# Optimization experiments

Hardware: AMD Instinct MI355X
Metric: run time of the kernel (lower is better)

## Reference

```python
import jax, jax.numpy as jnp
import numpy as np

HEAD_SIZE = 64
EPS_GN = 1e-5 * 8 * 8  # GroupNorm eps = 1e-5 * head_size_divisor**2


def rwkv7_scan(w_raw, q, k, v, a, b):
    """RWKV-7 'wind backstepping' linear recurrence.
    Inputs [B,T,H,N]. Per step (matching the CUDA kernel):
      decay = exp(-exp(w_raw)); sa = S @ a; S = S*decay + sa b^T + v k^T; y = S @ q
    State S is [B,H,N_value,N_key]."""
    decay = jnp.exp(-jnp.exp(w_raw))
    B, T, H, N = q.shape
    xs = tuple(jnp.moveaxis(t, 1, 0) for t in (decay, q, k, v, a, b))  # [T,B,H,N]
    S0 = jnp.zeros((B, H, N, N), q.dtype)

    def step(S, inp):
        d, qt, kt, vt, at, bt = inp
        sa = jnp.einsum('bhij,bhj->bhi', S, at)
        S = S * d[:, :, None, :] + sa[..., None] * bt[:, :, None, :] + vt[..., None] * kt[:, :, None, :]
        y = jnp.einsum('bhij,bhj->bhi', S, qt)
        return S, y

    _, ys = jax.lax.scan(step, S0, xs)
    return jnp.moveaxis(ys, 0, 1)  # [B,T,H,N]


def setup_inputs() -> dict:
    key = jax.random.key(0)
    B, T, C, H, N = 4, 960, 2048, 32, 64
    Dw, Da, Dv, Dg = 96, 96, 64, 256
    ks = iter(jax.random.split(key, 40))

    def nrm(shape, s=0.02):
        return jax.random.normal(next(ks), shape, jnp.float32) * s

    def uni(shape):
        return jax.random.uniform(next(ks), shape, jnp.float32)

    return dict(
        x=nrm((B, T, C), 1.0),
        v_first=nrm((B, T, C), 1.0),
        x_r=uni((1, 1, C)), x_w=uni((1, 1, C)), x_k=uni((1, 1, C)),
        x_v=uni((1, 1, C)), x_a=uni((1, 1, C)), x_g=uni((1, 1, C)),
        w0=jnp.linspace(-7.0, -2.0, C, dtype=jnp.float32).reshape(1, 1, C) + 0.5,
        w1=nrm((C, Dw)), w2=nrm((Dw, C)),
        a0=nrm((1, 1, C)), a1=nrm((C, Da)), a2=nrm((Da, C)),
        v0=jnp.ones((1, 1, C), jnp.float32), v1=nrm((C, Dv)), v2=nrm((Dv, C)),
        g1=nrm((C, Dg)), g2=nrm((Dg, C)),
        k_k=jnp.full((1, 1, C), 0.85, jnp.float32),
        k_a=jnp.ones((1, 1, C), jnp.float32),
        r_k=nrm((H, N)),
        Wr=nrm((C, C)), Wk=nrm((C, C)), Wv=nrm((C, C)), Wo=nrm((C, C)),
        ln_w=jnp.ones((C,), jnp.float32), ln_b=jnp.zeros((C,), jnp.float32),
    )


def reference(x, v_first, x_r, x_w, x_k, x_v, x_a, x_g,
              w0, w1, w2, a0, a1, a2, v0, v1, v2, g1, g2,
              k_k, k_a, r_k, Wr, Wk, Wv, Wo, ln_w, ln_b):
    B, T, C = x.shape
    H = C // HEAD_SIZE
    # time_shift: ZeroPad2d((0,0,1,-1)) == shift right by 1 along T with zero at t=0
    x_prev = jnp.pad(x, ((0, 0), (1, 0), (0, 0)))[:, :T]
    xx = x_prev - x
    xr = x + xx * x_r; xw = x + xx * x_w; xk = x + xx * x_k
    xv = x + xx * x_v; xa = x + xx * x_a; xg = x + xx * x_g

    r = xr @ Wr.T
    w = -jax.nn.softplus(-(w0 + jnp.tanh(xw @ w1) @ w2)) - 0.5
    k = xk @ Wk.T
    v = xv @ Wv.T
    # layer_id != 0: residual-value mixing with first layer's value
    v = v + (v_first - v) * jax.nn.sigmoid(v0 + (xv @ v1) @ v2)
    a = jax.nn.sigmoid(a0 + (xa @ a1) @ a2)
    g = jax.nn.sigmoid(xg @ g1) @ g2

    kk = (k * k_k).reshape(B, T, H, HEAD_SIZE)
    kk = kk / jnp.maximum(jnp.linalg.norm(kk, axis=-1, keepdims=True), 1e-12)  # F.normalize
    kk = kk.reshape(B, T, C)
    k = k * (1 + (a - 1) * k_a)

    hs = lambda t: t.reshape(B, T, H, HEAD_SIZE)
    y = rwkv7_scan(hs(w), hs(r), hs(k), hs(v), hs(-kk), hs(kk * a)).reshape(B, T, C)

    # GroupNorm(H groups over C)
    yg = y.reshape(B, T, H, HEAD_SIZE)
    mu = yg.mean(-1, keepdims=True)
    var = yg.var(-1, keepdims=True)
    y = ((yg - mu) / jnp.sqrt(var + EPS_GN)).reshape(B, T, C) * ln_w + ln_b

    y = y + ((hs(r) * hs(k) * r_k).sum(-1, keepdims=True) * hs(v)).reshape(B, T, C)
    return (y * g) @ Wo.T
```

## Files before the change

kernel.cpp:

```cpp
#include <hip/hip_runtime.h>
#include <stdint.h>

#define BDIM 4
#define TDIM 960
#define CDIM 2048
#define HDIM 32
#define NDIM 64
#define BT   (BDIM*TDIM)

typedef unsigned short u16;
typedef __attribute__((ext_vector_type(8))) short short8;
typedef __attribute__((ext_vector_type(4))) float f32x4;

__device__ __forceinline__ float b2f(u16 u){
  union{unsigned int i; float f;}x; x.i=((unsigned int)u)<<16; return x.f;
}
__device__ __forceinline__ u16 f2b(float f){
  union{float f; unsigned int i;}x; x.f=f;
  unsigned int r = x.i + 0x7fffu + ((x.i>>16)&1u);
  return (u16)(r>>16);
}
__device__ __forceinline__ void unpack8(uint4 p, float* o){
  o[0]=b2f((u16)(p.x&0xffff)); o[1]=b2f((u16)(p.x>>16));
  o[2]=b2f((u16)(p.y&0xffff)); o[3]=b2f((u16)(p.y>>16));
  o[4]=b2f((u16)(p.z&0xffff)); o[5]=b2f((u16)(p.z>>16));
  o[6]=b2f((u16)(p.w&0xffff)); o[7]=b2f((u16)(p.w>>16));
}
__device__ __forceinline__ uint4 pack8(const float* o){
  uint4 p;
  p.x = (unsigned)f2b(o[0]) | ((unsigned)f2b(o[1])<<16);
  p.y = (unsigned)f2b(o[2]) | ((unsigned)f2b(o[3])<<16);
  p.z = (unsigned)f2b(o[4]) | ((unsigned)f2b(o[5])<<16);
  p.w = (unsigned)f2b(o[6]) | ((unsigned)f2b(o[7])<<16);
  return p;
}
__device__ __forceinline__ void ld8f(const float* p, float* o){
  float4 a = *(const float4*)p;
  float4 b = *(const float4*)(p+4);
  o[0]=a.x;o[1]=a.y;o[2]=a.z;o[3]=a.w;o[4]=b.x;o[5]=b.y;o[6]=b.z;o[7]=b.w;
}
__device__ __forceinline__ float sigm(float x){ return 1.f/(1.f+expf(-x)); }
__device__ __forceinline__ void stc(float* p, float v){ *p = v; }
__device__ __forceinline__ void stc(u16* p, float v){ *p = f2b(v); }

__device__ __forceinline__ float row_red16(float x){
  x += __int_as_float(__builtin_amdgcn_update_dpp(0, __float_as_int(x), 0xB1,  0xF, 0xF, true));
  x += __int_as_float(__builtin_amdgcn_update_dpp(0, __float_as_int(x), 0x4E,  0xF, 0xF, true));
  x += __int_as_float(__builtin_amdgcn_update_dpp(0, __float_as_int(x), 0x141, 0xF, 0xF, true));
  x += __int_as_float(__builtin_amdgcn_update_dpp(0, __float_as_int(x), 0x140, 0xF, 0xF, true));
  return x;
}

__global__ __launch_bounds__(256) void cvt_kernel(const float* src, u16* dst){
  size_t i = ((size_t)blockIdx.x*256 + threadIdx.x)*8;
  float v[8]; ld8f(src+i, v);
  *(uint4*)(dst+i) = pack8(v);
}

struct TJob { const float* src; u16* dst; int R, Cs, DR, DC; };
struct TJobs8 { TJob j[8]; };

__global__ __launch_bounds__(256) void transpose_pad_kernel(TJobs8 jobs){
  TJob jb = jobs.j[blockIdx.z];
  int idx = blockIdx.x*256 + threadIdx.x;
  int total = jb.DR*jb.DC;
  if (idx >= total) return;
  int i = idx / jb.DC, k = idx % jb.DC;
  float v = 0.f;
  if (i < jb.Cs && k < jb.R) v = jb.src[(size_t)k*jb.Cs + i];
  jb.dst[idx] = f2b(v);
}

__global__ __launch_bounds__(256) void mix_kernel(
  const float* x,
  const float* cr, const float* cw, const float* ck,
  const float* cv, const float* ca, const float* cg,
  u16* mr, u16* mw, u16* mk, u16* mv, u16* ma, u16* mg)
{
  size_t tid = (size_t)blockIdx.x*256 + threadIdx.x;
  size_t base = tid*8;
  int c = (int)(base % CDIM);
  int row = (int)(base / CDIM);
  int t = row % TDIM;
  float xc[8], xp[8], xx[8], cf[8], o[8];
  ld8f(x+base, xc);
  if (t > 0) {
    ld8f(x+base-CDIM, xp);
  } else {
    for(int j=0;j<8;j++) xp[j]=0.f;
  }
  #pragma unroll
  for(int j=0;j<8;j++) xx[j]=xp[j]-xc[j];
#define DOMIX(CP, OP) do { ld8f(CP+c, cf); \
  _Pragma("unroll") for(int j=0;j<8;j++) o[j]=xc[j]+xx[j]*cf[j]; \
  *(uint4*)(OP+base)=pack8(o); } while(0)
  DOMIX(cr, mr); DOMIX(cw, mw); DOMIX(ck, mk);
  DOMIX(cv, mv); DOMIX(ca, ma); DOMIX(cg, mg);
#undef DOMIX
}

struct GemmJob {
  const u16* A; const u16* Bt; void* C;
  int nbm, nbn, K, lda, ldb, ldc;
};
struct GemmJobs { GemmJob j[4]; };

template<typename TC>
__global__ __launch_bounds__(256, 2) void gemm_bt_kernel(GemmJobs jobs){
  GemmJob jb = jobs.j[blockIdx.z];
  int bm = blockIdx.x % jb.nbm;
  int bn = blockIdx.x / jb.nbm;
  if (bn >= jb.nbn) return;
  __shared__ __attribute__((aligned(16))) u16 As[128*64];
  __shared__ __attribute__((aligned(16))) u16 Bs[128*64];
  int tid = threadIdx.x;
  int wave = tid>>6, lane = tid&63;
  int wr = wave>>1, wc = wave&1;
  f32x4 acc[4][4];
  #pragma unroll
  for(int i=0;i<4;i++)
    #pragma unroll
    for(int j=0;j<4;j++) acc[i][j] = (f32x4){0.f,0.f,0.f,0.f};
  const int rA0 = bm*128;
  const int rB0 = bn*128;
  int srow = (lane>>3);
  int scol = (lane&7)*8;
  for (int k0=0; k0<jb.K; k0+=64){
    #pragma unroll
    for (int it=0; it<4; ++it){
      int rr = wave*32 + it*8;
      const u16* gA = jb.A + (size_t)(rA0 + rr + srow)*jb.lda + (k0 + scol);
      __builtin_amdgcn_global_load_lds((const __attribute__((address_space(1))) void*)gA,
          (__attribute__((address_space(3))) void*)&As[rr*64], 16, 0, 0);
      const u16* gB = jb.Bt + (size_t)(rB0 + rr + srow)*jb.ldb + (k0 + scol);
      __builtin_amdgcn_global_load_lds((const __attribute__((address_space(1))) void*)gB,
          (__attribute__((address_space(3))) void*)&Bs[rr*64], 16, 0, 0);
    }
    __syncthreads();
    #pragma unroll
    for (int kc=0; kc<2; ++kc){
      short8 af[4], bfr[4];
      int ko = kc*32 + (lane>>4)*8;
      #pragma unroll
      for (int mi=0; mi<4; ++mi)
        af[mi] = *(const short8*)&As[(wr*64 + mi*16 + (lane&15))*64 + ko];
      #pragma unroll
      for (int ni=0; ni<4; ++ni)
        bfr[ni] = *(const short8*)&Bs[(wc*64 + ni*16 + (lane&15))*64 + ko];
      #pragma unroll
      for (int mi=0; mi<4; ++mi)
        #pragma unroll
        for (int ni=0; ni<4; ++ni)
          acc[mi][ni] = __builtin_amdgcn_mfma_f32_16x16x32_bf16(af[mi], bfr[ni], acc[mi][ni], 0, 0, 0);
    }
    __syncthreads();
  }
  TC* C = (TC*)jb.C;
  int cn = (lane&15);
  int rq = (lane>>4)*4;
  #pragma unroll
  for (int mi=0; mi<4; ++mi){
    #pragma unroll
    for (int ni=0; ni<4; ++ni){
      int col = rB0 + wc*64 + ni*16 + cn;
      int row = rA0 + wr*64 + mi*16 + rq;
      #pragma unroll
      for (int e=0; e<4; ++e)
        stc(&C[(size_t)(row+e)*jb.ldc + col], acc[mi][ni][e]);
    }
  }
}

__global__ __launch_bounds__(256) void act_kernel(u16* hw, u16* hg){
  int idx = blockIdx.x*256 + threadIdx.x;
  if (blockIdx.z==0){ if (idx < BT*128) hw[idx] = f2b(tanhf(b2f(hw[idx]))); }
  else              { if (idx < BT*256) hg[idx] = f2b(sigm(b2f(hg[idx]))); }
}

__global__ __launch_bounds__(256) void post_kernel(
  const u16* kbuf, const u16* vraw, const float* vfirst,
  const u16* wl, const u16* al, const u16* vl,
  const float* w0, const float* a0, const float* v0,
  const float* kkc, const float* kac,
  float* dout, u16* ks, u16* vs, u16* as_, u16* bs)
{
  int row = blockIdx.x, tid = threadIdx.x;
  int c = tid*8;
  size_t base = (size_t)row*CDIM + c;
  float kf[8], vr[8], vf[8], wlf[8], alf[8], vlf[8], w0f[8], a0f[8], v0f[8], kkf[8], kaf[8];
  unpack8(*(const uint4*)(kbuf+base), kf);
  unpack8(*(const uint4*)(vraw+base), vr);
  ld8f(vfirst+base, vf);
  unpack8(*(const uint4*)(wl+base), wlf);
  unpack8(*(const uint4*)(al+base), alf);
  unpack8(*(const uint4*)(vl+base), vlf);
  ld8f(w0+c, w0f);
  ld8f(a0+c, a0f);
  ld8f(v0+c, v0f);
  ld8f(kkc+c, kkf);
  ld8f(kac+c, kaf);
  float dv[8], av[8], vv[8], kkr[8], kfin[8], asv[8], bsv[8];
  float ssq = 0.f;
  #pragma unroll
  for (int j=0;j<8;j++){
    float wv = -log1pf(expf(-(w0f[j]+wlf[j]))) - 0.5f;
    dv[j]  = expf(-expf(wv));
    av[j]  = sigm(a0f[j]+alf[j]);
    vv[j]  = vr[j] + (vf[j]-vr[j])*sigm(v0f[j]+vlf[j]);
    kkr[j] = kf[j]*kkf[j];
    ssq   += kkr[j]*kkr[j];
    kfin[j]= kf[j]*(1.f + (av[j]-1.f)*kaf[j]);
  }
  ssq += __shfl_xor(ssq,1); ssq += __shfl_xor(ssq,2); ssq += __shfl_xor(ssq,4);
  float inv = 1.f/fmaxf(sqrtf(ssq), 1e-12f);
  #pragma unroll
  for (int j=0;j<8;j++){ float kkn = kkr[j]*inv; asv[j] = -kkn; bsv[j] = kkn*av[j]; }
  *(float4*)(dout+base)   = make_float4(dv[0],dv[1],dv[2],dv[3]);
  *(float4*)(dout+base+4) = make_float4(dv[4],dv[5],dv[6],dv[7]);
  *(uint4*)(ks+base)  = pack8(kfin);
  *(uint4*)(vs+base)  = pack8(vv);
  *(uint4*)(as_+base) = pack8(asv);
  *(uint4*)(bs+base)  = pack8(bsv);
}

__global__ __launch_bounds__(256, 2) void scan_kernel(
  const float* __restrict__ decayp, const u16* __restrict__ qb,
  const u16* __restrict__ kb, const u16* __restrict__ vb,
  const u16* __restrict__ ab, const u16* __restrict__ bb,
  float* __restrict__ yb)
{
  int blk = blockIdx.x;
  int b    = blk >> 7;
  int h    = (blk >> 2) & 31;
  int qtr  = blk & 3;
  int tid = threadIdx.x;
  int jg = tid & 15;
  int ii = tid >> 4;
  int row = qtr*16 + ii;
  size_t hbase = ((size_t)b*TDIM)*CDIM + (size_t)h*NDIM;

  const float* dp = decayp + hbase + jg*4;
  const u16*  qp = qb + hbase + jg*4;
  const u16*  kp = kb + hbase + jg*4;
  const u16*  ap = ab + hbase + jg*4;
  const u16*  bp = bb + hbase + jg*4;
  const u16*  vp = vb + hbase + row;

  float S[4] = {0.f, 0.f, 0.f, 0.f};

  struct StepRegs { f32x4 d; ushort4 q, k, a, b; u16 v; };
  auto loadstep = [&](int t)->StepRegs{
    StepRegs r;
    size_t off = (size_t)t*CDIM;
    r.d = *(const f32x4*)(dp + off);
    r.q = *(const ushort4*)(qp + off);
    r.k = *(const ushort4*)(kp + off);
    r.a = *(const ushort4*)(ap + off);
    r.b = *(const ushort4*)(bp + off);
    r.v = vp[off];
    return r;
  };
  auto dostep = [&](const StepRegs& r)->float{
    float a0=b2f(r.a.x), a1=b2f(r.a.y), a2=b2f(r.a.z), a3=b2f(r.a.w);
    float sap = (S[0]*a0 + S[1]*a1) + (S[2]*a2 + S[3]*a3);
    sap = row_red16(sap);
    float k0=b2f(r.k.x), k1=b2f(r.k.y), k2=b2f(r.k.z), k3=b2f(r.k.w);
    float c0=b2f(r.b.x), c1=b2f(r.b.y), c2=b2f(r.b.z), c3=b2f(r.b.w);
    float vi=b2f(r.v);
    S[0] = S[0]*r.d[0] + sap*c0 + vi*k0;
    S[1] = S[1]*r.d[1] + sap*c1 + vi*k1;
    S[2] = S[2]*r.d[2] + sap*c2 + vi*k2;
    S[3] = S[3]*r.d[3] + sap*c3 + vi*k3;
    return (S[0]*b2f(r.q.x) + S[1]*b2f(r.q.y)) + (S[2]*b2f(r.q.z) + S[3]*b2f(r.q.w));
  };

  StepRegs R0 = loadstep(0), R1 = loadstep(1), R2 = loadstep(2), R3 = loadstep(3);
  for (int g=0; g<120; ++g){
    float yp[8];
#define STEP(RR, S_) { int t_ = g*8 + (S_); int tn_ = t_+4 < TDIM ? t_+4 : TDIM-1; \
    StepRegs nn_ = loadstep(tn_); yp[S_] = dostep(RR); RR = nn_; }
    STEP(R0,0) STEP(R1,1) STEP(R2,2) STEP(R3,3)
    STEP(R0,4) STEP(R1,5) STEP(R2,6) STEP(R3,7)
#undef STEP
    #pragma unroll
    for (int s=0; s<8; ++s) yp[s] = row_red16(yp[s]);
    if (jg < 8){
      float out = 0.f;
      #pragma unroll
      for (int s=0; s<8; ++s) if (jg==s) out = yp[s];
      yb[hbase + (size_t)(g*8+jg)*CDIM + row] = out;
    }
  }
}

__global__ __launch_bounds__(256) void final_kernel(
  const float* yb, const u16* rb, const u16* ks, const u16* vs,
  const float* rk, const float* lnw, const float* lnb, const u16* gl, u16* yg)
{
  int row = blockIdx.x, tid = threadIdx.x;
  int c = tid*8;
  size_t base = (size_t)row*CDIM + c;
  float y[8], rf[8], kf[8], vf[8], rkf[8], lw[8], lb[8], gf[8];
  ld8f(yb+base, y);
  unpack8(*(const uint4*)(rb+base), rf);
  unpack8(*(const uint4*)(ks+base), kf);
  unpack8(*(const uint4*)(vs+base), vf);
  ld8f(rk+c,  rkf);
  ld8f(lnw+c, lw);
  ld8f(lnb+c, lb);
  unpack8(*(const uint4*)(gl+base), gf);
  float sy=0.f, syy=0.f, coef=0.f;
  #pragma unroll
  for (int j=0;j<8;j++){ sy+=y[j]; syy+=y[j]*y[j]; coef += rf[j]*kf[j]*rkf[j]; }
  sy  += __shfl_xor(sy,1);  sy  += __shfl_xor(sy,2);  sy  += __shfl_xor(sy,4);
  syy += __shfl_xor(syy,1); syy += __shfl_xor(syy,2); syy += __shfl_xor(syy,4);
  coef+= __shfl_xor(coef,1);coef+= __shfl_xor(coef,2);coef+= __shfl_xor(coef,4);
  float mu  = sy*(1.f/64.f);
  float var = syy*(1.f/64.f) - mu*mu;
  float rs  = rsqrtf(var + 6.4e-4f);
  float o[8];
  #pragma unroll
  for (int j=0;j<8;j++)
    o[j] = (((y[j]-mu)*rs)*lw[j] + lb[j] + coef*vf[j]) * gf[j];
  *(uint4*)(yg+base) = pack8(o);
}

extern "C" void kernel_launch(void* const* d_in, const int* in_sizes, int n_in,
                              void* d_out, int out_size, void* d_ws, size_t ws_size,
                              hipStream_t stream)
{
  const float* x      = (const float*)d_in[0];
  const float* vfirst = (const float*)d_in[1];
  const float* c_r = (const float*)d_in[2];
  const float* c_w = (const float*)d_in[3];
  const float* c_k = (const float*)d_in[4];
  const float* c_v = (const float*)d_in[5];
  const float* c_a = (const float*)d_in[6];
  const float* c_g = (const float*)d_in[7];
  const float* w0i = (const float*)d_in[8];
  const float* w1i = (const float*)d_in[9];
  const float* w2i = (const float*)d_in[10];
  const float* a0i = (const float*)d_in[11];
  const float* a1i = (const float*)d_in[12];
  const float* a2i = (const float*)d_in[13];
  const float* v0i = (const float*)d_in[14];
  const float* v1i = (const float*)d_in[15];
  const float* v2i = (const float*)d_in[16];
  const float* g1i = (const float*)d_in[17];
  const float* g2i = (const float*)d_in[18];
  const float* kki = (const float*)d_in[19];
  const float* kai = (const float*)d_in[20];
  const float* rki = (const float*)d_in[21];
  const float* Wr  = (const float*)d_in[22];
  const float* Wk  = (const float*)d_in[23];
  const float* Wv  = (const float*)d_in[24];
  const float* Wo  = (const float*)d_in[25];
  const float* lnw = (const float*)d_in[26];
  const float* lnb = (const float*)d_in[27];

  char* ws = (char*)d_ws;
  const size_t S2 = (size_t)BT*CDIM*2;
  u16* MIXR = (u16*)(ws + 0*S2);
  u16* MIXW = (u16*)(ws + 1*S2);
  u16* MIXK = (u16*)(ws + 2*S2);
  u16* MIXV = (u16*)(ws + 3*S2);
  u16* MIXA = (u16*)(ws + 4*S2);
  u16* MIXG = (u16*)(ws + 5*S2);
  u16* RBUF = (u16*)(ws + 6*S2);
  u16* KBUF = (u16*)(ws + 7*S2);
  u16* VRAW = (u16*)(ws + 8*S2);
  char* WB = ws + 9*S2;
  u16* WSLOT = (u16*)WB;
  char* WT = WB + 8388608;
  u16* W1T = (u16*)(WT + 0);
  u16* A1T = (u16*)(WT + 524288);
  u16* V1T = (u16*)(WT + 1048576);
  u16* G1T = (u16*)(WT + 1572864);
  u16* W2T = (u16*)(WT + 2621440);
  u16* A2T = (u16*)(WT + 3145728);
  u16* V2T = (u16*)(WT + 3670016);
  u16* G2T = (u16*)(WT + 4194304);
  char* HB = WT + 5242880;
  u16* HW = (u16*)(HB + 0);
  u16* HA = (u16*)(HB + 983040);
  u16* HV = (u16*)(HB + 1966080);
  u16* HG = (u16*)(HB + 2949120);
  char* L2 = HB + 4915200;
  u16* WL = (u16*)(L2 + 0*S2);
  u16* AL = (u16*)(L2 + 1*S2);
  u16* VL = (u16*)(L2 + 2*S2);
  u16* GL = (u16*)(L2 + 3*S2);
  float* WDEC = (float*)(ws + 0*S2);
  u16* KS = (u16*)(ws + 2*S2);
  u16* VS = (u16*)(ws + 3*S2);
  u16* AS = (u16*)(ws + 4*S2);
  u16* BS = (u16*)(ws + 5*S2);
  float* YBUF = (float*)(L2 + 0*S2);
  u16* YG = (u16*)(L2 + 2*S2);
  (void)in_sizes; (void)n_in; (void)out_size; (void)ws_size;

  TJobs8 tj;
  tj.j[0] = (TJob){w1i, W1T, 2048,  96, 128, 2048};
  tj.j[1] = (TJob){a1i, A1T, 2048,  96, 128, 2048};
  tj.j[2] = (TJob){v1i, V1T, 2048,  64, 128, 2048};
  tj.j[3] = (TJob){g1i, G1T, 2048, 256, 256, 2048};
  tj.j[4] = (TJob){w2i, W2T,   96, 2048, 2048, 128};
  tj.j[5] = (TJob){a2i, A2T,   96, 2048, 2048, 128};
  tj.j[6] = (TJob){v2i, V2T,   64, 2048, 2048, 128};
  tj.j[7] = (TJob){g2i, G2T,  256, 2048, 2048, 256};
  transpose_pad_kernel<<<dim3(2048,1,8), 256, 0, stream>>>(tj);

  mix_kernel<<<dim3(BT*CDIM/8/256), 256, 0, stream>>>(
      x, c_r, c_w, c_k, c_v, c_a, c_g, MIXR, MIXW, MIXK, MIXV, MIXA, MIXG);

  {
    GemmJobs gj;
    cvt_kernel<<<dim3(2048), 256, 0, stream>>>(Wr, WSLOT);
    gj.j[0] = (GemmJob){MIXR, WSLOT, RBUF, 30, 16, 2048, 2048, 2048, 2048};
    gj.j[1] = gj.j[0]; gj.j[2] = gj.j[0]; gj.j[3] = gj.j[0];
    gemm_bt_kernel<u16><<<dim3(480,1,1), 256, 0, stream>>>(gj);
    cvt_kernel<<<dim3(2048), 256, 0, stream>>>(Wk, WSLOT);
    gj.j[0] = (GemmJob){MIXK, WSLOT, KBUF, 30, 16, 2048, 2048, 2048, 2048};
    gemm_bt_kernel<u16><<<dim3(480,1,1), 256, 0, stream>>>(gj);
    cvt_kernel<<<dim3(2048), 256, 0, stream>>>(Wv, WSLOT);
    gj.j[0] = (GemmJob){MIXV, WSLOT, VRAW, 30, 16, 2048, 2048, 2048, 2048};
    gemm_bt_kernel<u16><<<dim3(480,1,1), 256, 0, stream>>>(gj);
  }

  GemmJobs lj1;
  lj1.j[0] = (GemmJob){MIXW, W1T, HW, 30, 1, 2048, 2048, 2048, 128};
  lj1.j[1] = (GemmJob){MIXA, A1T, HA, 30, 1, 2048, 2048, 2048, 128};
  lj1.j[2] = (GemmJob){MIXV, V1T, HV, 30, 1, 2048, 2048, 2048, 128};
  lj1.j[3] = (GemmJob){MIXG, G1T, HG, 30, 2, 2048, 2048, 2048, 256};
  gemm_bt_kernel<u16><<<dim3(60,1,4), 256, 0, stream>>>(lj1);

  act_kernel<<<dim3(3840,1,2), 256, 0, stream>>>(HW, HG);

  GemmJobs lj2;
  lj2.j[0] = (GemmJob){HW, W2T, WL, 30, 16, 128, 128, 128, 2048};
  lj2.j[1] = (GemmJob){HA, A2T, AL, 30, 16, 128, 128, 128, 2048};
  lj2.j[2] = (GemmJob){HV, V2T, VL, 30, 16, 128, 128, 128, 2048};
  lj2.j[3] = (GemmJob){HG, G2T, GL, 30, 16, 256, 256, 256, 2048};
  gemm_bt_kernel<u16><<<dim3(480,1,4), 256, 0, stream>>>(lj2);

  post_kernel<<<dim3(BT), 256, 0, stream>>>(
      KBUF, VRAW, vfirst, WL, AL, VL, w0i, a0i, v0i, kki, kai,
      WDEC, KS, VS, AS, BS);

  scan_kernel<<<dim3(512), 256, 0, stream>>>(
      WDEC, RBUF, KS, VS, AS, BS, YBUF);

  final_kernel<<<dim3(BT), 256, 0, stream>>>(
      YBUF, RBUF, KS, VS, rki, lnw, lnb, GL, YG);

  cvt_kernel<<<dim3(2048), 256, 0, stream>>>(Wo, WSLOT);
  GemmJobs oj;
  oj.j[0] = (GemmJob){YG, WSLOT, d_out, 30, 16, 2048, 2048, 2048, 2048};
  oj.j[1] = oj.j[0]; oj.j[2] = oj.j[0]; oj.j[3] = oj.j[0];
  gemm_bt_kernel<float><<<dim3(480,1,1), 256, 0, stream>>>(oj);
}
```

Baseline: 897.7 us.

## Split scan state across 32 lanes per row and interleave a/b vectors

The scan kernel now gives each thread two state columns instead of four, with 32 lanes per state row and 8 rows per block. The grid doubles to 1024 blocks and occupancy is raised to 4 blocks per CU. The a and b vectors are written by post_kernel in an interleaved layout, so one 8-byte load fetches both. This shortens the serial per-step work and exposes more parallelism in the latency-bound recurrence, at the cost of an extra cross-half shuffle per reduction and more redundant loads of the shared vectors.

```diff
diff --git a/kernel.cpp b/kernel.cpp
--- a/kernel.cpp
+++ b/kernel.cpp
@@ -182,7 +182,7 @@
   const u16* wl, const u16* al, const u16* vl,
   const float* w0, const float* a0, const float* v0,
   const float* kkc, const float* kac,
-  float* dout, u16* ks, u16* vs, u16* as_, u16* bs)
+  float* dout, u16* ks, u16* vs, uint2* abi)
 {
   int row = blockIdx.x, tid = threadIdx.x;
   int c = tid*8;
@@ -219,59 +219,62 @@
   *(float4*)(dout+base+4) = make_float4(dv[4],dv[5],dv[6],dv[7]);
   *(uint4*)(ks+base)  = pack8(kfin);
   *(uint4*)(vs+base)  = pack8(vv);
-  *(uint4*)(as_+base) = pack8(asv);
-  *(uint4*)(bs+base)  = pack8(bsv);
-}
-
-__global__ __launch_bounds__(256, 2) void scan_kernel(
+  uint2* abe = abi + (size_t)row*1024 + (size_t)(c>>6)*32 + ((c&63)>>1);
+  #pragma unroll
+  for (int m=0;m<4;m++)
+    abe[m] = make_uint2((unsigned)f2b(asv[2*m]) | ((unsigned)f2b(asv[2*m+1])<<16),
+                        (unsigned)f2b(bsv[2*m]) | ((unsigned)f2b(bsv[2*m+1])<<16));
+}
+
+__global__ __launch_bounds__(256, 4) void scan_kernel(
   const float* __restrict__ decayp, const u16* __restrict__ qb,
   const u16* __restrict__ kb, const u16* __restrict__ vb,
-  const u16* __restrict__ ab, const u16* __restrict__ bb,
-  float* __restrict__ yb)
+  const uint2* __restrict__ abi, float* __restrict__ yb)
 {
   int blk = blockIdx.x;
-  int b    = blk >> 7;
-  int h    = (blk >> 2) & 31;
-  int qtr  = blk & 3;
+  int b   = blk >> 8;
+  int h   = (blk >> 3) & 31;
+  int oct = blk & 7;
   int tid = threadIdx.x;
-  int jg = tid & 15;
-  int ii = tid >> 4;
-  int row = qtr*16 + ii;
+  int jg  = tid & 31;
+  int ii  = tid >> 5;
+  int row = oct*8 + ii;
   size_t hbase = ((size_t)b*TDIM)*CDIM + (size_t)h*NDIM;
 
-  const float* dp = decayp + hbase + jg*4;
-  const u16*  qp = qb + hbase + jg*4;
-  const u16*  kp = kb + hbase + jg*4;
-  const u16*  ap = ab + hbase + jg*4;
-  const u16*  bp = bb + hbase + jg*4;
-  const u16*  vp = vb + hbase + row;
-
-  float S[4] = {0.f, 0.f, 0.f, 0.f};
-
-  struct StepRegs { f32x4 d; ushort4 q, k, a, b; u16 v; };
+  const char* dU = (const char*)(decayp + hbase);
+  const char* qU = (const char*)(qb + hbase);
+  const char* kU = (const char*)(kb + hbase);
+  const char* vU = (const char*)(vb + hbase);
+  const char* aU = (const char*)(abi + (size_t)b*TDIM*1024 + (size_t)h*32);
+
+  unsigned o8 = (unsigned)(jg*8);
+  unsigned o4 = (unsigned)(jg*4);
+  unsigned ov = (unsigned)(row*2);
+
+  float Sx = 0.f, Sy = 0.f;
+
+  struct StepRegs { float2 d; uint2 ab; unsigned q, k; u16 v; };
   auto loadstep = [&](int t)->StepRegs{
     StepRegs r;
-    size_t off = (size_t)t*CDIM;
-    r.d = *(const f32x4*)(dp + off);
-    r.q = *(const ushort4*)(qp + off);
-    r.k = *(const ushort4*)(kp + off);
-    r.a = *(const ushort4*)(ap + off);
-    r.b = *(const ushort4*)(bp + off);
-    r.v = vp[off];
+    unsigned t8 = (unsigned)t*8192u, t4 = (unsigned)t*4096u;
+    r.d  = *(const float2*)  (dU + (o8 + t8));
+    r.ab = *(const uint2*)   (aU + (o8 + t8));
+    r.q  = *(const unsigned*)(qU + (o4 + t4));
+    r.k  = *(const unsigned*)(kU + (o4 + t4));
+    r.v  = *(const u16*)     (vU + (ov + t4));
     return r;
   };
   auto dostep = [&](const StepRegs& r)->float{
-    float a0=b2f(r.a.x), a1=b2f(r.a.y), a2=b2f(r.a.z), a3=b2f(r.a.w);
-    float sap = (S[0]*a0 + S[1]*a1) + (S[2]*a2 + S[3]*a3);
+    float aLo = b2f((u16)(r.ab.x & 0xffff)), aHi = b2f((u16)(r.ab.x >> 16));
+    float sap = Sx*aLo + Sy*aHi;
     sap = row_red16(sap);
-    float k0=b2f(r.k.x), k1=b2f(r.k.y), k2=b2f(r.k.z), k3=b2f(r.k.w);
-    float c0=b2f(r.b.x), c1=b2f(r.b.y), c2=b2f(r.b.z), c3=b2f(r.b.w);
-    float vi=b2f(r.v);
-    S[0] = S[0]*r.d[0] + sap*c0 + vi*k0;
-    S[1] = S[1]*r.d[1] + sap*c1 + vi*k1;
-    S[2] = S[2]*r.d[2] + sap*c2 + vi*k2;
-    S[3] = S[3]*r.d[3] + sap*c3 + vi*k3;
-    return (S[0]*b2f(r.q.x) + S[1]*b2f(r.q.y)) + (S[2]*b2f(r.q.z) + S[3]*b2f(r.q.w));
+    sap += __shfl_xor(sap, 16);
+    float bLo = b2f((u16)(r.ab.y & 0xffff)), bHi = b2f((u16)(r.ab.y >> 16));
+    float kLo = b2f((u16)(r.k & 0xffff)),    kHi = b2f((u16)(r.k >> 16));
+    float vi  = b2f(r.v);
+    Sx = Sx*r.d.x + sap*bLo + vi*kLo;
+    Sy = Sy*r.d.y + sap*bHi + vi*kHi;
+    return Sx*b2f((u16)(r.q & 0xffff)) + Sy*b2f((u16)(r.q >> 16));
   };
 
   StepRegs R0 = loadstep(0), R1 = loadstep(1), R2 = loadstep(2), R3 = loadstep(3);
@@ -283,7 +286,10 @@
     STEP(R0,4) STEP(R1,5) STEP(R2,6) STEP(R3,7)
 #undef STEP
     #pragma unroll
-    for (int s=0; s<8; ++s) yp[s] = row_red16(yp[s]);
+    for (int s=0; s<8; ++s){
+      yp[s] = row_red16(yp[s]);
+      yp[s] += __shfl_xor(yp[s], 16);
+    }
     if (jg < 8){
       float out = 0.f;
       #pragma unroll
@@ -393,8 +399,7 @@
   float* WDEC = (float*)(ws + 0*S2);
   u16* KS = (u16*)(ws + 2*S2);
   u16* VS = (u16*)(ws + 3*S2);
-  u16* AS = (u16*)(ws + 4*S2);
-  u16* BS = (u16*)(ws + 5*S2);
+  uint2* ABI = (uint2*)(ws + 4*S2);
   float* YBUF = (float*)(L2 + 0*S2);
   u16* YG = (u16*)(L2 + 2*S2);
   (void)in_sizes; (void)n_in; (void)out_size; (void)ws_size;
@@ -445,10 +450,10 @@
 
   post_kernel<<<dim3(BT), 256, 0, stream>>>(
       KBUF, VRAW, vfirst, WL, AL, VL, w0i, a0i, v0i, kki, kai,
-      WDEC, KS, VS, AS, BS);
-
-  scan_kernel<<<dim3(512), 256, 0, stream>>>(
-      WDEC, RBUF, KS, VS, AS, BS, YBUF);
+      WDEC, KS, VS, ABI);
+
+  scan_kernel<<<dim3(1024), 256, 0, stream>>>(
+      WDEC, RBUF, KS, VS, ABI, YBUF);
 
   final_kernel<<<dim3(BT), 256, 0, stream>>>(
       YBUF, RBUF, KS, VS, rki, lnw, lnb, GL, YG);
```

Result: slower. 932.7 us (+3.9%).

## Interleave q/k and a/b into packed buffers and deepen scan prefetch

Applied to the files above, without the earlier changes.

The post kernel now writes q and k interleaved into one buffer and a and b into another, so each scan step issues fewer, wider loads (two 16-byte loads instead of four 8-byte loads). The scan prefetch depth grows from 4 to 8 steps, and sched_barriers split each 8-step group into pairs of steps. The final kernel reads r and k from the interleaved buffer. The aim is to cut load instruction count and hide latency in the serial scan, at the cost of more registers and an extra r read in post_kernel.

```diff
diff --git a/kernel.cpp b/kernel.cpp
--- a/kernel.cpp
+++ b/kernel.cpp
@@ -20,6 +20,9 @@
   unsigned int r = x.i + 0x7fffu + ((x.i>>16)&1u);
   return (u16)(r>>16);
 }
+__device__ __forceinline__ unsigned pk2(float lo, float hi){
+  return (unsigned)f2b(lo) | ((unsigned)f2b(hi)<<16);
+}
 __device__ __forceinline__ void unpack8(uint4 p, float* o){
   o[0]=b2f((u16)(p.x&0xffff)); o[1]=b2f((u16)(p.x>>16));
   o[2]=b2f((u16)(p.y&0xffff)); o[3]=b2f((u16)(p.y>>16));
@@ -28,10 +31,10 @@
 }
 __device__ __forceinline__ uint4 pack8(const float* o){
   uint4 p;
-  p.x = (unsigned)f2b(o[0]) | ((unsigned)f2b(o[1])<<16);
-  p.y = (unsigned)f2b(o[2]) | ((unsigned)f2b(o[3])<<16);
-  p.z = (unsigned)f2b(o[4]) | ((unsigned)f2b(o[5])<<16);
-  p.w = (unsigned)f2b(o[6]) | ((unsigned)f2b(o[7])<<16);
+  p.x = pk2(o[0],o[1]);
+  p.y = pk2(o[2],o[3]);
+  p.z = pk2(o[4],o[5]);
+  p.w = pk2(o[6],o[7]);
   return p;
 }
 __device__ __forceinline__ void ld8f(const float* p, float* o){
@@ -178,16 +181,17 @@
 }
 
 __global__ __launch_bounds__(256) void post_kernel(
-  const u16* kbuf, const u16* vraw, const float* vfirst,
+  const u16* rbuf, const u16* kbuf, const u16* vraw, const float* vfirst,
   const u16* wl, const u16* al, const u16* vl,
   const float* w0, const float* a0, const float* v0,
   const float* kkc, const float* kac,
-  float* dout, u16* ks, u16* vs, u16* as_, u16* bs)
+  float* dout, uint4* qki, uint4* abi, u16* vs)
 {
   int row = blockIdx.x, tid = threadIdx.x;
   int c = tid*8;
   size_t base = (size_t)row*CDIM + c;
-  float kf[8], vr[8], vf[8], wlf[8], alf[8], vlf[8], w0f[8], a0f[8], v0f[8], kkf[8], kaf[8];
+  float qf[8], kf[8], vr[8], vf[8], wlf[8], alf[8], vlf[8], w0f[8], a0f[8], v0f[8], kkf[8], kaf[8];
+  unpack8(*(const uint4*)(rbuf+base), qf);
   unpack8(*(const uint4*)(kbuf+base), kf);
   unpack8(*(const uint4*)(vraw+base), vr);
   ld8f(vfirst+base, vf);
@@ -217,84 +221,87 @@
   for (int j=0;j<8;j++){ float kkn = kkr[j]*inv; asv[j] = -kkn; bsv[j] = kkn*av[j]; }
   *(float4*)(dout+base)   = make_float4(dv[0],dv[1],dv[2],dv[3]);
   *(float4*)(dout+base+4) = make_float4(dv[4],dv[5],dv[6],dv[7]);
-  *(uint4*)(ks+base)  = pack8(kfin);
-  *(uint4*)(vs+base)  = pack8(vv);
-  *(uint4*)(as_+base) = pack8(asv);
-  *(uint4*)(bs+base)  = pack8(bsv);
+  uint4* qke = (uint4*)((char*)qki + (size_t)row*8192 + (size_t)c*4);
+  qke[0] = make_uint4(pk2(qf[0],qf[1]), pk2(kfin[0],kfin[1]), pk2(qf[2],qf[3]), pk2(kfin[2],kfin[3]));
+  qke[1] = make_uint4(pk2(qf[4],qf[5]), pk2(kfin[4],kfin[5]), pk2(qf[6],qf[7]), pk2(kfin[6],kfin[7]));
+  uint4* abe = (uint4*)((char*)abi + (size_t)row*8192 + (size_t)c*4);
+  abe[0] = make_uint4(pk2(asv[0],asv[1]), pk2(bsv[0],bsv[1]), pk2(asv[2],asv[3]), pk2(bsv[2],bsv[3]));
+  abe[1] = make_uint4(pk2(asv[4],asv[5]), pk2(bsv[4],bsv[5]), pk2(asv[6],asv[7]), pk2(bsv[6],bsv[7]));
+  *(uint4*)(vs+base) = pack8(vv);
 }
 
 __global__ __launch_bounds__(256, 2) void scan_kernel(
-  const float* __restrict__ decayp, const u16* __restrict__ qb,
-  const u16* __restrict__ kb, const u16* __restrict__ vb,
-  const u16* __restrict__ ab, const u16* __restrict__ bb,
+  const float* __restrict__ decayp, const uint4* __restrict__ qki,
+  const uint4* __restrict__ abi, const u16* __restrict__ vs,
   float* __restrict__ yb)
 {
   int blk = blockIdx.x;
   int b    = blk >> 7;
   int h    = (blk >> 2) & 31;
   int qtr  = blk & 3;
-  int tid = threadIdx.x;
-  int jg = tid & 15;
-  int ii = tid >> 4;
-  int row = qtr*16 + ii;
-  size_t hbase = ((size_t)b*TDIM)*CDIM + (size_t)h*NDIM;
-
-  const float* dp = decayp + hbase + jg*4;
-  const u16*  qp = qb + hbase + jg*4;
-  const u16*  kp = kb + hbase + jg*4;
-  const u16*  ap = ab + hbase + jg*4;
-  const u16*  bp = bb + hbase + jg*4;
-  const u16*  vp = vb + hbase + row;
-
-  float S[4] = {0.f, 0.f, 0.f, 0.f};
-
-  struct StepRegs { f32x4 d; ushort4 q, k, a, b; u16 v; };
-  auto loadstep = [&](int t)->StepRegs{
-    StepRegs r;
-    size_t off = (size_t)t*CDIM;
-    r.d = *(const f32x4*)(dp + off);
-    r.q = *(const ushort4*)(qp + off);
-    r.k = *(const ushort4*)(kp + off);
-    r.a = *(const ushort4*)(ap + off);
-    r.b = *(const ushort4*)(bp + off);
-    r.v = vp[off];
+  int tid  = threadIdx.x;
+  int jg   = tid & 15;
+  int ii   = tid >> 4;
+  int row  = qtr*16 + ii;
+
+  const char* dP = (const char*)decayp + (size_t)b*TDIM*8192 + h*256 + jg*16;
+  const char* qP = (const char*)qki    + (size_t)b*TDIM*8192 + h*256 + jg*16;
+  const char* aP = (const char*)abi    + (size_t)b*TDIM*8192 + h*256 + jg*16;
+  const char* vP = (const char*)vs     + (size_t)b*TDIM*4096 + h*128 + row*2;
+
+  float S0=0.f, S1=0.f, S2=0.f, S3=0.f;
+
+  struct SR { f32x4 d; uint4 qk; uint4 ab; u16 v; };
+  auto ld = [&](int t)->SR{
+    SR r; size_t o = (size_t)t*8192;
+    r.d  = *(const f32x4*)(dP + o);
+    r.qk = *(const uint4*)(qP + o);
+    r.ab = *(const uint4*)(aP + o);
+    r.v  = *(const u16*)(vP + (size_t)t*4096);
     return r;
   };
-  auto dostep = [&](const StepRegs& r)->float{
-    float a0=b2f(r.a.x), a1=b2f(r.a.y), a2=b2f(r.a.z), a3=b2f(r.a.w);
-    float sap = (S[0]*a0 + S[1]*a1) + (S[2]*a2 + S[3]*a3);
+  auto dostep = [&](const SR& r)->float{
+    float a0=b2f((u16)(r.ab.x&0xffff)), a1=b2f((u16)(r.ab.x>>16));
+    float a2=b2f((u16)(r.ab.z&0xffff)), a3=b2f((u16)(r.ab.z>>16));
+    float sap = (S0*a0 + S1*a1) + (S2*a2 + S3*a3);
     sap = row_red16(sap);
-    float k0=b2f(r.k.x), k1=b2f(r.k.y), k2=b2f(r.k.z), k3=b2f(r.k.w);
-    float c0=b2f(r.b.x), c1=b2f(r.b.y), c2=b2f(r.b.z), c3=b2f(r.b.w);
+    float c0=b2f((u16)(r.ab.y&0xffff)), c1=b2f((u16)(r.ab.y>>16));
+    float c2=b2f((u16)(r.ab.w&0xffff)), c3=b2f((u16)(r.ab.w>>16));
+    float k0=b2f((u16)(r.qk.y&0xffff)), k1=b2f((u16)(r.qk.y>>16));
+    float k2=b2f((u16)(r.qk.w&0xffff)), k3=b2f((u16)(r.qk.w>>16));
     float vi=b2f(r.v);
-    S[0] = S[0]*r.d[0] + sap*c0 + vi*k0;
-    S[1] = S[1]*r.d[1] + sap*c1 + vi*k1;
-    S[2] = S[2]*r.d[2] + sap*c2 + vi*k2;
-    S[3] = S[3]*r.d[3] + sap*c3 + vi*k3;
-    return (S[0]*b2f(r.q.x) + S[1]*b2f(r.q.y)) + (S[2]*b2f(r.q.z) + S[3]*b2f(r.q.w));
+    S0 = S0*r.d[0] + sap*c0 + vi*k0;
+    S1 = S1*r.d[1] + sap*c1 + vi*k1;
+    S2 = S2*r.d[2] + sap*c2 + vi*k2;
+    S3 = S3*r.d[3] + sap*c3 + vi*k3;
+    return (S0*b2f((u16)(r.qk.x&0xffff)) + S1*b2f((u16)(r.qk.x>>16)))
+         + (S2*b2f((u16)(r.qk.z&0xffff)) + S3*b2f((u16)(r.qk.z>>16)));
   };
 
-  StepRegs R0 = loadstep(0), R1 = loadstep(1), R2 = loadstep(2), R3 = loadstep(3);
+  SR A0=ld(0), A1=ld(1), A2=ld(2), A3=ld(3), A4=ld(4), A5=ld(5), A6=ld(6), A7=ld(7);
   for (int g=0; g<120; ++g){
+    int tn = g*8 + 8;
     float yp[8];
-#define STEP(RR, S_) { int t_ = g*8 + (S_); int tn_ = t_+4 < TDIM ? t_+4 : TDIM-1; \
-    StepRegs nn_ = loadstep(tn_); yp[S_] = dostep(RR); RR = nn_; }
-    STEP(R0,0) STEP(R1,1) STEP(R2,2) STEP(R3,3)
-    STEP(R0,4) STEP(R1,5) STEP(R2,6) STEP(R3,7)
-#undef STEP
+#define STEPR(AR, S_) { yp[S_] = dostep(AR); int t_ = tn + (S_); \
+    AR = ld(t_ < TDIM ? t_ : TDIM-1); }
+    STEPR(A0,0) STEPR(A1,1) __builtin_amdgcn_sched_barrier(0);
+    STEPR(A2,2) STEPR(A3,3) __builtin_amdgcn_sched_barrier(0);
+    STEPR(A4,4) STEPR(A5,5) __builtin_amdgcn_sched_barrier(0);
+    STEPR(A6,6) STEPR(A7,7) __builtin_amdgcn_sched_barrier(0);
+#undef STEPR
     #pragma unroll
     for (int s=0; s<8; ++s) yp[s] = row_red16(yp[s]);
     if (jg < 8){
       float out = 0.f;
       #pragma unroll
       for (int s=0; s<8; ++s) if (jg==s) out = yp[s];
-      yb[hbase + (size_t)(g*8+jg)*CDIM + row] = out;
+      yb[(size_t)b*TDIM*CDIM + (size_t)(g*8+jg)*CDIM + h*NDIM + row] = out;
     }
   }
 }
 
 __global__ __launch_bounds__(256) void final_kernel(
-  const float* yb, const u16* rb, const u16* ks, const u16* vs,
+  const float* yb, const uint4* qki, const u16* vs,
   const float* rk, const float* lnw, const float* lnb, const u16* gl, u16* yg)
 {
   int row = blockIdx.x, tid = threadIdx.x;
@@ -302,8 +309,16 @@
   size_t base = (size_t)row*CDIM + c;
   float y[8], rf[8], kf[8], vf[8], rkf[8], lw[8], lb[8], gf[8];
   ld8f(yb+base, y);
-  unpack8(*(const uint4*)(rb+base), rf);
-  unpack8(*(const uint4*)(ks+base), kf);
+  const uint4* qke = (const uint4*)((const char*)qki + (size_t)row*8192 + (size_t)c*4);
+  uint4 e0 = qke[0], e1 = qke[1];
+  rf[0]=b2f((u16)(e0.x&0xffff)); rf[1]=b2f((u16)(e0.x>>16));
+  rf[2]=b2f((u16)(e0.z&0xffff)); rf[3]=b2f((u16)(e0.z>>16));
+  rf[4]=b2f((u16)(e1.x&0xffff)); rf[5]=b2f((u16)(e1.x>>16));
+  rf[6]=b2f((u16)(e1.z&0xffff)); rf[7]=b2f((u16)(e1.z>>16));
+  kf[0]=b2f((u16)(e0.y&0xffff)); kf[1]=b2f((u16)(e0.y>>16));
+  kf[2]=b2f((u16)(e0.w&0xffff)); kf[3]=b2f((u16)(e0.w>>16));
+  kf[4]=b2f((u16)(e1.y&0xffff)); kf[5]=b2f((u16)(e1.y>>16));
+  kf[6]=b2f((u16)(e1.w&0xffff)); kf[7]=b2f((u16)(e1.w>>16));
   unpack8(*(const uint4*)(vs+base), vf);
   ld8f(rk+c,  rkf);
   ld8f(lnw+c, lw);
@@ -391,10 +406,9 @@
   u16* VL = (u16*)(L2 + 2*S2);
   u16* GL = (u16*)(L2 + 3*S2);
   float* WDEC = (float*)(ws + 0*S2);
-  u16* KS = (u16*)(ws + 2*S2);
-  u16* VS = (u16*)(ws + 3*S2);
-  u16* AS = (u16*)(ws + 4*S2);
-  u16* BS = (u16*)(ws + 5*S2);
+  uint4* QKI  = (uint4*)(ws + 2*S2);
+  uint4* ABI  = (uint4*)(ws + 4*S2);
+  u16*   VS6  = (u16*)(ws + 6*S2);
   float* YBUF = (float*)(L2 + 0*S2);
   u16* YG = (u16*)(L2 + 2*S2);
   (void)in_sizes; (void)n_in; (void)out_size; (void)ws_size;
@@ -444,14 +458,14 @@
   gemm_bt_kernel<u16><<<dim3(480,1,4), 256, 0, stream>>>(lj2);
 
   post_kernel<<<dim3(BT), 256, 0, stream>>>(
-      KBUF, VRAW, vfirst, WL, AL, VL, w0i, a0i, v0i, kki, kai,
-      WDEC, KS, VS, AS, BS);
+      RBUF, KBUF, VRAW, vfirst, WL, AL, VL, w0i, a0i, v0i, kki, kai,
+      WDEC, QKI, ABI, VS6);
 
   scan_kernel<<<dim3(512), 256, 0, stream>>>(
-      WDEC, RBUF, KS, VS, AS, BS, YBUF);
+      WDEC, QKI, ABI, VS6, YBUF);
 
   final_kernel<<<dim3(BT), 256, 0, stream>>>(
-      YBUF, RBUF, KS, VS, rki, lnw, lnb, GL, YG);
+      YBUF, QKI, VS6, rki, lnw, lnb, GL, YG);
 
   cvt_kernel<<<dim3(2048), 256, 0, stream>>>(Wo, WSLOT);
   GemmJobs oj;
```

Measured after the change: 823.3 us. 8.3% less time.
